# Optimization experiments

Measured on AMD Instinct MI355X. Metric: run time of the kernel, lower is better.

The kernel has to match this reference:

```python
import jax, jax.numpy as jnp
import numpy as np

# Physical constants from the source (is_low_resistance=True branch)
V_REF = 0.25
G_MIN = 0.1
G_MAX = 1.0
N_AVG = 2.18
N_STD = 0.115

B, N_IN, N_OUT = 64, 1024, 1024


def setup_inputs() -> dict:
    key = jax.random.key(0)
    k0, k1, k2, k3 = jax.random.split(key, 4)
    stdv = 1.0 / np.sqrt(N_IN)
    x = jax.random.normal(k0, (B, N_IN), jnp.float32)
    # RandomNormal(mean=0.5, stddev=1/sqrt(n_in)) per build()
    w_pos = 0.5 + stdv * jax.random.normal(k1, (N_IN, N_OUT), jnp.float32)
    w_neg = 0.5 + stdv * jax.random.normal(k2, (N_IN, N_OUT), jnp.float32)
    b_pos = jnp.full((N_OUT,), 0.5, jnp.float32)
    b_neg = jnp.full((N_OUT,), 0.5, jnp.float32)
    # Per-device nonlinearity parameter n ~ N(n_avg, n_std), one per crossbar cell
    n_param = N_AVG + N_STD * jax.random.normal(k3, (N_IN + 1, 2 * N_OUT), jnp.float32)
    return {"x": x, "w_pos": w_pos, "w_neg": w_neg, "b_pos": b_pos, "b_neg": b_neg, "n_param": n_param}


def reference(x, w_pos, w_neg, b_pos, b_neg, n_param):
    # Fold biases into the weight matrix; interleave pos/neg columns -> [n_in+1, 2*n_out]
    W_pos = jnp.concatenate([w_pos, b_pos[None, :]], axis=0)
    W_neg = jnp.concatenate([w_neg, b_neg[None, :]], axis=0)
    W = jnp.stack([W_pos, W_neg], axis=-1).reshape(W_pos.shape[0], -1)
    # Append ones column to inputs -> [B, n_in+1]
    inputs = jnp.concatenate([x, jnp.ones((x.shape[0], 1), x.dtype)], axis=1)

    max_w = jnp.max(jnp.abs(W))
    k_G = (G_MAX - G_MIN) / max_w
    # w_params_to_G (differential scheme): proportional mapping with G_min offset
    G = G_MIN + k_G * W  # [n_in+1, 2*n_out]
    # x_to_V: V = k_V * x with k_V = 2*V_ref
    k_V = 2.0 * V_REF
    V = k_V * inputs  # [B, n_in+1]

    # Nonlinear parameterized I-V: I = sign(V) * V_ref * G * (|V|/V_ref)^log2(n)
    exponent = jnp.log2(n_param)  # [n_in+1, 2*n_out]
    sign = jnp.sign(V)[:, :, None]
    ratio = (jnp.abs(V) / V_REF)[:, :, None]
    I_ind = sign * V_REF * G[None] * ratio ** exponent[None]  # [B, n_in+1, 2*n_out]
    I = jnp.sum(I_ind, axis=1)  # bit-line currents [B, 2*n_out]

    # I_to_y (differential): subtract interleaved neg columns, undo k_V/k_G scaling
    y = (I[:, 0::2] - I[:, 1::2]) / (k_V * k_G)  # [B, n_out]
    return y
```

## Files before the change

kernel.cpp:

```cpp
#include <hip/hip_runtime.h>

#define NB 64
#define NI 1024
#define NO 1024
#define IROWS (NI + 1)
#define S_SPLIT 32
#define TJ 64
#define NOUT (NB * NO)

__device__ __forceinline__ float fast_exp2(float x) { return __builtin_amdgcn_exp2f(x); }
__device__ __forceinline__ float fast_log2(float x) { return __builtin_amdgcn_logf(x); }

__global__ __launch_bounds__(256) void maxabs_kernel(
    const float* __restrict__ wp, const float* __restrict__ wn,
    const float* __restrict__ bp, const float* __restrict__ bn,
    unsigned* __restrict__ maxbits)
{
    int tid = blockIdx.x * blockDim.x + threadIdx.x;
    int stride = gridDim.x * blockDim.x;
    float m = 0.0f;
    const int NW = NI * NO;
    for (int idx = tid; idx < NW; idx += stride) {
        m = fmaxf(m, fabsf(wp[idx]));
        m = fmaxf(m, fabsf(wn[idx]));
    }
    for (int idx = tid; idx < NO; idx += stride) {
        m = fmaxf(m, fabsf(bp[idx]));
        m = fmaxf(m, fabsf(bn[idx]));
    }
    #pragma unroll
    for (int off = 32; off > 0; off >>= 1)
        m = fmaxf(m, __shfl_xor(m, off));
    if ((threadIdx.x & 63) == 0)
        atomicMax(maxbits, __float_as_uint(m));
}

__global__ __launch_bounds__(256) void memristor_main(
    const float* __restrict__ x,
    const float* __restrict__ w_pos, const float* __restrict__ w_neg,
    const float* __restrict__ b_pos, const float* __restrict__ b_neg,
    const float* __restrict__ n_param,
    const unsigned* __restrict__ maxbits,
    float* __restrict__ partial)
{
    __shared__ float2 LS[NB][33];

    const float maxw = __uint_as_float(*maxbits);
    const float k_G = 0.9f / maxw;

    const int jt = blockIdx.x;
    const int s  = blockIdx.y;
    const int base  = IROWS / S_SPLIT;
    const int extra = IROWS % S_SPLIT;
    const int i0  = s * base + min(s, extra);
    const int len = base + (s < extra ? 1 : 0);

    const int tid = threadIdx.x;

    {
        const int li = tid & 63;
        if (li < len) {
            const int gi = i0 + li;
            #pragma unroll 4
            for (int bb = tid >> 6; bb < NB; bb += 4) {
                float v  = (gi < NI) ? x[bb * NI + gi] : 1.0f;
                float sg = (v > 0.0f) ? 1.0f : ((v < 0.0f) ? -1.0f : 0.0f);
                float L  = fast_log2(fabsf(v)) + 1.0f;
                LS[bb][li] = make_float2(L, sg);
            }
        }
    }
    __syncthreads();

    const int tx = tid & 63;
    const int ty = tid >> 6;
    const int jp = jt * TJ + tx;

    float acc[16];
    #pragma unroll
    for (int k = 0; k < 16; ++k) acc[k] = 0.0f;

    const int reg_len = min(len, NI - i0);
    for (int ii = 0; ii < reg_len; ++ii) {
        const int gi = i0 + ii;
        const float  wpv = w_pos[gi * NO + jp];
        const float  wnv = w_neg[gi * NO + jp];
        const float2 n2  = reinterpret_cast<const float2*>(n_param + (size_t)gi * 2 * NO)[jp];
        const float Gp = fmaf(k_G, wpv, 0.1f);
        const float Gn = fmaf(k_G, wnv, 0.1f);
        const float ep = fast_log2(n2.x);
        const float en = fast_log2(n2.y);
        #pragma unroll
        for (int k = 0; k < 16; ++k) {
            const float2 ls = LS[ty * 16 + k][ii];
            const float Pp = fast_exp2(ep * ls.x);
            const float Pn = fast_exp2(en * ls.x);
            const float u  = fmaf(Gn, -Pn, Gp * Pp);
            acc[k] = fmaf(ls.y, u, acc[k]);
        }
    }

    if (i0 + len > NI) {
        const int ii = len - 1;
        const float  wpv = b_pos[jp];
        const float  wnv = b_neg[jp];
        const float2 n2  = reinterpret_cast<const float2*>(n_param + (size_t)NI * 2 * NO)[jp];
        const float Gp = fmaf(k_G, wpv, 0.1f);
        const float Gn = fmaf(k_G, wnv, 0.1f);
        const float ep = fast_log2(n2.x);
        const float en = fast_log2(n2.y);
        #pragma unroll
        for (int k = 0; k < 16; ++k) {
            const float2 ls = LS[ty * 16 + k][ii];
            const float Pp = fast_exp2(ep * ls.x);
            const float Pn = fast_exp2(en * ls.x);
            const float u  = fmaf(Gn, -Pn, Gp * Pp);
            acc[k] = fmaf(ls.y, u, acc[k]);
        }
    }

    float* slice = partial + (size_t)s * NOUT;
    #pragma unroll
    for (int k = 0; k < 16; ++k)
        slice[(ty * 16 + k) * NO + jp] = acc[k];
}

__global__ __launch_bounds__(256) void reduce_kernel(
    const float* __restrict__ partial,
    const unsigned* __restrict__ maxbits,
    float* __restrict__ y)
{
    const int o = blockIdx.x * 256 + threadIdx.x;
    float sum = 0.0f;
    #pragma unroll
    for (int p = 0; p < S_SPLIT; ++p)
        sum += partial[(size_t)p * NOUT + o];
    const float maxw = __uint_as_float(*maxbits);
    y[o] = sum * (0.5f * maxw / 0.9f);
}

extern "C" void kernel_launch(void* const* d_in, const int* in_sizes, int n_in,
                              void* d_out, int out_size, void* d_ws, size_t ws_size,
                              hipStream_t stream)
{
    const float* x     = (const float*)d_in[0];
    const float* w_pos = (const float*)d_in[1];
    const float* w_neg = (const float*)d_in[2];
    const float* b_pos = (const float*)d_in[3];
    const float* b_neg = (const float*)d_in[4];
    const float* n_par = (const float*)d_in[5];
    float*    y        = (float*)d_out;

    float*    partial  = (float*)d_ws;
    unsigned* maxbits  = (unsigned*)((char*)d_ws + (size_t)S_SPLIT * NOUT * sizeof(float));

    (void)hipMemsetAsync(maxbits, 0, sizeof(unsigned), stream);

    maxabs_kernel<<<256, 256, 0, stream>>>(w_pos, w_neg, b_pos, b_neg, maxbits);

    dim3 grid(NO / TJ, S_SPLIT);
    memristor_main<<<grid, 256, 0, stream>>>(x, w_pos, w_neg, b_pos, b_neg, n_par,
                                             maxbits, partial);

    reduce_kernel<<<NOUT / 256, 256, 0, stream>>>(partial, maxbits, y);
}
```

Measured before the change: 130.0 us.

## Fold conductance into exponent and replace atomic max with per-block partials

The inner loop now computes G*ratio^e as exp2(e*L + log2 G) by precomputing log2 of the conductance per row. This removes a multiply per term and lets the difference become a plain subtract. The global max is now written as 256 per-block partial maxima, read and reduced by each consumer block, which drops the memset and the atomics. The max pass also uses float4 loads. Folding G into the exponent can add a little rounding error, and every consumer block now pays a small extra reduction and a barrier.

```diff
diff --git a/kernel.cpp b/kernel.cpp
--- a/kernel.cpp
+++ b/kernel.cpp
@@ -7,32 +7,46 @@
 #define S_SPLIT 32
 #define TJ 64
 #define NOUT (NB * NO)
+#define MAXBLK 256
 
 __device__ __forceinline__ float fast_exp2(float x) { return __builtin_amdgcn_exp2f(x); }
 __device__ __forceinline__ float fast_log2(float x) { return __builtin_amdgcn_logf(x); }
 
-__global__ __launch_bounds__(256) void maxabs_kernel(
-    const float* __restrict__ wp, const float* __restrict__ wn,
+__global__ __launch_bounds__(256) void maxabs_stage(
+    const float4* __restrict__ wp4, const float4* __restrict__ wn4,
     const float* __restrict__ bp, const float* __restrict__ bn,
-    unsigned* __restrict__ maxbits)
+    float* __restrict__ ws_max)
 {
-    int tid = blockIdx.x * blockDim.x + threadIdx.x;
-    int stride = gridDim.x * blockDim.x;
+    const int tid = blockIdx.x * 256 + threadIdx.x;
+    const int NW4 = NI * NO / 4;
     float m = 0.0f;
-    const int NW = NI * NO;
-    for (int idx = tid; idx < NW; idx += stride) {
-        m = fmaxf(m, fabsf(wp[idx]));
-        m = fmaxf(m, fabsf(wn[idx]));
+    for (int idx = tid; idx < NW4; idx += MAXBLK * 256) {
+        float4 a = wp4[idx], b = wn4[idx];
+        m = fmaxf(m, fmaxf(fmaxf(fabsf(a.x), fabsf(a.y)), fmaxf(fabsf(a.z), fabsf(a.w))));
+        m = fmaxf(m, fmaxf(fmaxf(fabsf(b.x), fabsf(b.y)), fmaxf(fabsf(b.z), fabsf(b.w))));
     }
-    for (int idx = tid; idx < NO; idx += stride) {
-        m = fmaxf(m, fabsf(bp[idx]));
-        m = fmaxf(m, fabsf(bn[idx]));
-    }
+    if (tid < NO) m = fmaxf(m, fmaxf(fabsf(bp[tid]), fabsf(bn[tid])));
+
     #pragma unroll
     for (int off = 32; off > 0; off >>= 1)
         m = fmaxf(m, __shfl_xor(m, off));
-    if ((threadIdx.x & 63) == 0)
-        atomicMax(maxbits, __float_as_uint(m));
+    __shared__ float wm[4];
+    if ((threadIdx.x & 63) == 0) wm[threadIdx.x >> 6] = m;
+    __syncthreads();
+    if (threadIdx.x == 0)
+        ws_max[blockIdx.x] = fmaxf(fmaxf(wm[0], wm[1]), fmaxf(wm[2], wm[3]));
+}
+
+__device__ __forceinline__ float block_maxw(const float* __restrict__ ws_max, int tid)
+{
+    float m = ws_max[tid & 255];
+    #pragma unroll
+    for (int off = 32; off > 0; off >>= 1)
+        m = fmaxf(m, __shfl_xor(m, off));
+    __shared__ float wm[4];
+    if ((tid & 63) == 0) wm[tid >> 6] = m;
+    __syncthreads();
+    return fmaxf(fmaxf(wm[0], wm[1]), fmaxf(wm[2], wm[3]));
 }
 
 __global__ __launch_bounds__(256) void memristor_main(
@@ -40,13 +54,14 @@
     const float* __restrict__ w_pos, const float* __restrict__ w_neg,
     const float* __restrict__ b_pos, const float* __restrict__ b_neg,
     const float* __restrict__ n_param,
-    const unsigned* __restrict__ maxbits,
+    const float* __restrict__ ws_max,
     float* __restrict__ partial)
 {
+    const int tid = threadIdx.x;
+    const float maxw = block_maxw(ws_max, tid);
+    const float k_G = 0.9f / maxw;
+
     __shared__ float2 LS[NB][33];
-
-    const float maxw = __uint_as_float(*maxbits);
-    const float k_G = 0.9f / maxw;
 
     const int jt = blockIdx.x;
     const int s  = blockIdx.y;
@@ -54,8 +69,6 @@
     const int extra = IROWS % S_SPLIT;
     const int i0  = s * base + min(s, extra);
     const int len = base + (s < extra ? 1 : 0);
-
-    const int tid = threadIdx.x;
 
     {
         const int li = tid & 63;
@@ -83,39 +96,33 @@
     const int reg_len = min(len, NI - i0);
     for (int ii = 0; ii < reg_len; ++ii) {
         const int gi = i0 + ii;
-        const float  wpv = w_pos[gi * NO + jp];
-        const float  wnv = w_neg[gi * NO + jp];
-        const float2 n2  = reinterpret_cast<const float2*>(n_param + (size_t)gi * 2 * NO)[jp];
-        const float Gp = fmaf(k_G, wpv, 0.1f);
-        const float Gn = fmaf(k_G, wnv, 0.1f);
-        const float ep = fast_log2(n2.x);
-        const float en = fast_log2(n2.y);
+        const float2 n2 = reinterpret_cast<const float2*>(n_param + (size_t)gi * 2 * NO)[jp];
+        const float ep   = fast_log2(n2.x);
+        const float en   = fast_log2(n2.y);
+        const float lgGp = fast_log2(fmaf(k_G, w_pos[gi * NO + jp], 0.1f));
+        const float lgGn = fast_log2(fmaf(k_G, w_neg[gi * NO + jp], 0.1f));
         #pragma unroll
         for (int k = 0; k < 16; ++k) {
             const float2 ls = LS[ty * 16 + k][ii];
-            const float Pp = fast_exp2(ep * ls.x);
-            const float Pn = fast_exp2(en * ls.x);
-            const float u  = fmaf(Gn, -Pn, Gp * Pp);
-            acc[k] = fmaf(ls.y, u, acc[k]);
+            const float Pp = fast_exp2(fmaf(ep, ls.x, lgGp));
+            const float Pn = fast_exp2(fmaf(en, ls.x, lgGn));
+            acc[k] = fmaf(ls.y, Pp - Pn, acc[k]);
         }
     }
 
     if (i0 + len > NI) {
         const int ii = len - 1;
-        const float  wpv = b_pos[jp];
-        const float  wnv = b_neg[jp];
-        const float2 n2  = reinterpret_cast<const float2*>(n_param + (size_t)NI * 2 * NO)[jp];
-        const float Gp = fmaf(k_G, wpv, 0.1f);
-        const float Gn = fmaf(k_G, wnv, 0.1f);
-        const float ep = fast_log2(n2.x);
-        const float en = fast_log2(n2.y);
+        const float2 n2 = reinterpret_cast<const float2*>(n_param + (size_t)NI * 2 * NO)[jp];
+        const float ep   = fast_log2(n2.x);
+        const float en   = fast_log2(n2.y);
+        const float lgGp = fast_log2(fmaf(k_G, b_pos[jp], 0.1f));
+        const float lgGn = fast_log2(fmaf(k_G, b_neg[jp], 0.1f));
         #pragma unroll
         for (int k = 0; k < 16; ++k) {
             const float2 ls = LS[ty * 16 + k][ii];
-            const float Pp = fast_exp2(ep * ls.x);
-            const float Pn = fast_exp2(en * ls.x);
-            const float u  = fmaf(Gn, -Pn, Gp * Pp);
-            acc[k] = fmaf(ls.y, u, acc[k]);
+            const float Pp = fast_exp2(fmaf(ep, ls.x, lgGp));
+            const float Pn = fast_exp2(fmaf(en, ls.x, lgGn));
+            acc[k] = fmaf(ls.y, Pp - Pn, acc[k]);
         }
     }
 
@@ -127,15 +134,16 @@
 
 __global__ __launch_bounds__(256) void reduce_kernel(
     const float* __restrict__ partial,
-    const unsigned* __restrict__ maxbits,
+    const float* __restrict__ ws_max,
     float* __restrict__ y)
 {
-    const int o = blockIdx.x * 256 + threadIdx.x;
+    const int tid = threadIdx.x;
+    const float maxw = block_maxw(ws_max, tid);
+    const int o = blockIdx.x * 256 + tid;
     float sum = 0.0f;
     #pragma unroll
     for (int p = 0; p < S_SPLIT; ++p)
         sum += partial[(size_t)p * NOUT + o];
-    const float maxw = __uint_as_float(*maxbits);
     y[o] = sum * (0.5f * maxw / 0.9f);
 }
 
@@ -151,16 +159,15 @@
     const float* n_par = (const float*)d_in[5];
     float*    y        = (float*)d_out;
 
-    float*    partial  = (float*)d_ws;
-    unsigned* maxbits  = (unsigned*)((char*)d_ws + (size_t)S_SPLIT * NOUT * sizeof(float));
+    float* ws_max  = (float*)d_ws;
+    float* partial = (float*)d_ws + 1024;
 
-    (void)hipMemsetAsync(maxbits, 0, sizeof(unsigned), stream);
-
-    maxabs_kernel<<<256, 256, 0, stream>>>(w_pos, w_neg, b_pos, b_neg, maxbits);
+    maxabs_stage<<<MAXBLK, 256, 0, stream>>>(
+        (const float4*)w_pos, (const float4*)w_neg, b_pos, b_neg, ws_max);
 
     dim3 grid(NO / TJ, S_SPLIT);
     memristor_main<<<grid, 256, 0, stream>>>(x, w_pos, w_neg, b_pos, b_neg, n_par,
-                                             maxbits, partial);
+                                             ws_max, partial);
 
-    reduce_kernel<<<NOUT / 256, 256, 0, stream>>>(partial, maxbits, y);
+    reduce_kernel<<<NOUT / 256, 256, 0, stream>>>(partial, ws_max, y);
 }
```

New measurement: 108.0 us. 1.2x faster.
